# Kernel tuning notes

Measured on AMD Instinct MI355X. Metric: run time of the kernel, lower is better.

The kernel has to match this reference:

```python
import jax, jax.numpy as jnp
import numpy as np

R = 0.9  # compression ratio from init_kwargs


def _dct_matrix(N):
    """Orthonormal DCT-II matrix C of shape [N, N].
    (C @ v) along the last axis equals dct(v, norm='ortho').
    Its transpose is the orthonormal DCT-III (inverse)."""
    n = jnp.arange(N, dtype=jnp.float32)
    k = n[:, None]
    C = jnp.cos(jnp.pi * (2.0 * n[None, :] + 1.0) * k / (2.0 * N))
    s = jnp.full((N,), jnp.sqrt(2.0 / N), dtype=jnp.float32).at[0].set(jnp.sqrt(1.0 / N))
    return s[:, None] * C


def setup_inputs() -> dict:
    key = jax.random.key(0)
    # hidden states [B, T, D]
    x = jax.random.normal(key, (64, 1024, 768), dtype=jnp.float32)
    return {"x": x}


def reference(x):
    """CompressedModel.compress_hidden_state with compress_method='dct' and
    use_compressed_hidden_state=True:
      1) DCT-II (ortho) along the token axis T
      2) keep the first k = ceil(r*T) coefficients
      3) inverse DCT (ortho, size k) to reconstruct a shorter sequence
    Returns (x_reconstructed [B,k,D], x_dct [B,k,D]) matching dc_transform."""
    B, T, D = x.shape
    k = int(np.ceil(R * T))  # static under jit
    C_T = _dct_matrix(T)          # [T, T]
    # DCT along tokens, truncate to low-frequency k coeffs
    x_dct = jnp.einsum('kt,btd->bkd', C_T, x)[:, :k, :]  # [B, k, D]
    # inverse DCT of size k (DCT-III ortho = transpose of DCT-II ortho)
    C_k = _dct_matrix(k)          # [k, k]
    x_rec = jnp.einsum('mn,bmd->bnd', C_k, x_dct)         # [B, k, D]
    return x_rec, x_dct
```

## Files before the change

### kernel.cpp

```cpp
#include <hip/hip_runtime.h>
#include <hip/hip_bf16.h>

typedef __attribute__((ext_vector_type(8))) short short8;
typedef __attribute__((ext_vector_type(4))) float f32x4;

#define T_LEN   1024
#define KKEEP   922
#define DDIM    768
#define NBATCH  64

#define BM 128
#define BN 128
#define BK 32
#define LDSK 40

__global__ void gen_C1(__hip_bfloat16* __restrict__ C1) {
    int idx = blockIdx.x * 256 + threadIdx.x;
    if (idx >= 1024 * 1024) return;
    int kk = idx >> 10;
    int t  = idx & 1023;
    float val = 0.0f;
    if (kk < KKEEP) {
        float a1 = 3.14159265358979323846f * (2.0f * (float)t + 1.0f);
        float a2 = a1 * (float)kk;
        float a3 = a2 / 2048.0f;
        float s  = (kk == 0) ? sqrtf(1.0f / 1024.0f) : sqrtf(2.0f / 1024.0f);
        val = s * cosf(a3);
    }
    C1[idx] = __float2bfloat16(val);
}

__global__ void gen_C2T(__hip_bfloat16* __restrict__ A2) {
    int idx = blockIdx.x * 256 + threadIdx.x;
    if (idx >= 1024 * 928) return;
    int n = idx / 928;
    int m = idx - n * 928;
    float val = 0.0f;
    if (n < KKEEP && m < KKEEP) {
        float a1 = 3.14159265358979323846f * (2.0f * (float)n + 1.0f);
        float a2 = a1 * (float)m;
        float a3 = a2 / 1844.0f;
        float s  = (m == 0) ? sqrtf(1.0f / 922.0f) : sqrtf(2.0f / 922.0f);
        val = s * cosf(a3);
    }
    A2[idx] = __float2bfloat16(val);
}

__global__ __launch_bounds__(256)
void gemm_dct(const __hip_bfloat16* __restrict__ A, int lda, int ksteps,
              const float* __restrict__ B, int bRows, long long bStride,
              float* __restrict__ C, long long cStride)
{
    __shared__ __hip_bfloat16 As[2][BM * LDSK];
    __shared__ __hip_bfloat16 Bs[2][BN * LDSK];

    const int tid   = threadIdx.x;
    const int mBase = blockIdx.y * BM;
    const int nBase = blockIdx.x * BN;

    const float* __restrict__ Bb = B + (long long)blockIdx.z * bStride;
    float* __restrict__       Cb = C + (long long)blockIdx.z * cStride;

    auto stageA = [&](int buf, int k0) {
        int r = tid >> 1, half = tid & 1;
        const uint4* src = (const uint4*)(A + (size_t)(mBase + r) * lda + k0 + half * 16);
        uint4 v0 = src[0], v1 = src[1];
        uint4* dst = (uint4*)&As[buf][r * LDSK + half * 16];
        dst[0] = v0; dst[1] = v1;
    };
    auto stageB = [&](int buf, int k0) {
        #pragma unroll
        for (int p = 0; p < 4; ++p) {
            int idx = p * 256 + tid;
            int k   = idx & 31;
            int n4  = (idx >> 5) * 4;
            int gk  = k0 + k;
            float4 v = make_float4(0.f, 0.f, 0.f, 0.f);
            if (gk < bRows) v = *(const float4*)(Bb + (size_t)gk * DDIM + nBase + n4);
            __hip_bfloat16* d = &Bs[buf][n4 * LDSK + k];
            d[0 * LDSK] = __float2bfloat16(v.x);
            d[1 * LDSK] = __float2bfloat16(v.y);
            d[2 * LDSK] = __float2bfloat16(v.z);
            d[3 * LDSK] = __float2bfloat16(v.w);
        }
    };

    const int lane = tid & 63;
    const int wid  = tid >> 6;
    const int wm   = (wid >> 1) * 64;
    const int wn   = (wid & 1) * 64;
    const int lr   = lane & 15;
    const int g8   = (lane >> 4) * 8;

    f32x4 acc[4][4] = {};

    stageA(0, 0);
    stageB(0, 0);
    __syncthreads();

    for (int s = 0; s < ksteps; ++s) {
        int buf = s & 1;
        if (s + 1 < ksteps) {
            stageA(buf ^ 1, (s + 1) * BK);
            stageB(buf ^ 1, (s + 1) * BK);
        }
        short8 af[4], bfr[4];
        #pragma unroll
        for (int m = 0; m < 4; ++m)
            af[m] = *(const short8*)&As[buf][(wm + m * 16 + lr) * LDSK + g8];
        #pragma unroll
        for (int n = 0; n < 4; ++n)
            bfr[n] = *(const short8*)&Bs[buf][(wn + n * 16 + lr) * LDSK + g8];
        #pragma unroll
        for (int m = 0; m < 4; ++m)
            #pragma unroll
            for (int n = 0; n < 4; ++n)
                acc[m][n] = __builtin_amdgcn_mfma_f32_16x16x32_bf16(af[m], bfr[n], acc[m][n], 0, 0, 0);
        __syncthreads();
    }

    #pragma unroll
    for (int m = 0; m < 4; ++m) {
        int row0 = mBase + wm + m * 16 + (lane >> 4) * 4;
        #pragma unroll
        for (int n = 0; n < 4; ++n) {
            int col = nBase + wn + n * 16 + lr;
            #pragma unroll
            for (int i = 0; i < 4; ++i) {
                int row = row0 + i;
                if (row < KKEEP)
                    Cb[(size_t)row * DDIM + col] = acc[m][n][i];
            }
        }
    }
}

extern "C" void kernel_launch(void* const* d_in, const int* in_sizes, int n_in,
                              void* d_out, int out_size, void* d_ws, size_t ws_size,
                              hipStream_t stream)
{
    const float* x = (const float*)d_in[0];
    float* out  = (float*)d_out;
    float* xrec = out;
    float* xdct = out + (size_t)NBATCH * KKEEP * DDIM;

    __hip_bfloat16* C1 = (__hip_bfloat16*)d_ws;
    __hip_bfloat16* A2 = (__hip_bfloat16*)d_ws + 1024 * 1024;

    gen_C1<<<(1024 * 1024 + 255) / 256, 256, 0, stream>>>(C1);
    gen_C2T<<<(1024 * 928 + 255) / 256, 256, 0, stream>>>(A2);

    dim3 grid(DDIM / BN, 1024 / BM, NBATCH);

    gemm_dct<<<grid, 256, 0, stream>>>(C1, 1024, 32,
                                       x, T_LEN, (long long)T_LEN * DDIM,
                                       xdct, (long long)KKEEP * DDIM);

    gemm_dct<<<grid, 256, 0, stream>>>(A2, 928, 29,
                                       xdct, KKEEP, (long long)KKEEP * DDIM,
                                       xrec, (long long)KKEEP * DDIM);
}
```

Baseline: 976.8 us.

## Pre-transpose inputs to bf16 and use direct global-to-LDS loads in GEMM

Adds a transpose-and-convert kernel that writes x (and xdct when workspace allows) as bf16 in K-contiguous layout, using the xrec output buffer as scratch. A new GEMM then stages both operands with global_load_lds 16-byte transfers into unpadded LDS, replacing the per-element fp32-to-bf16 strided stores inside the main loop. The aim is to cut staging overhead and global traffic in the GEMM, at the price of extra transpose passes. The unpadded LDS layout may also cause bank conflicts.

Measured after the change: 791.0 us. 1.23x faster.

```diff
diff --git a/kernel.cpp b/kernel.cpp
--- a/kernel.cpp
+++ b/kernel.cpp
@@ -9,10 +9,6 @@
 #define DDIM    768
 #define NBATCH  64
 
-#define BM 128
-#define BN 128
-#define BK 32
-#define LDSK 40
 
 __global__ void gen_C1(__hip_bfloat16* __restrict__ C1) {
     int idx = blockIdx.x * 256 + threadIdx.x;
@@ -47,17 +43,124 @@
 }
 
 __global__ __launch_bounds__(256)
+void transpose_cvt(const float* __restrict__ in, __hip_bfloat16* __restrict__ out,
+                   int R, int C, int Rp)
+{
+    __shared__ float tile[64][65];
+    const int r0 = blockIdx.x * 64, c0 = blockIdx.y * 64, z = blockIdx.z;
+    const float* inz = in + (size_t)z * R * C;
+    __hip_bfloat16* outz = out + (size_t)z * C * Rp;
+    const int tid = threadIdx.x;
+    const int lr = tid >> 4, lc4 = (tid & 15) * 4;
+    #pragma unroll
+    for (int i = 0; i < 4; ++i) {
+        int row = i * 16 + lr;
+        int gr  = r0 + row;
+        float4 v = make_float4(0.f, 0.f, 0.f, 0.f);
+        if (gr < R) v = *(const float4*)(inz + (size_t)gr * C + c0 + lc4);
+        tile[row][lc4 + 0] = v.x; tile[row][lc4 + 1] = v.y;
+        tile[row][lc4 + 2] = v.z; tile[row][lc4 + 3] = v.w;
+    }
+    __syncthreads();
+    const int orow = tid >> 2, seg = tid & 3;
+    const int rB = r0 + seg * 16;
+    if (rB < Rp) {
+        alignas(16) __hip_bfloat16 tmp[16];
+        #pragma unroll
+        for (int j = 0; j < 16; ++j)
+            tmp[j] = __float2bfloat16(tile[seg * 16 + j][orow]);
+        uint4* dst = (uint4*)(outz + (size_t)(c0 + orow) * Rp + rB);
+        dst[0] = ((const uint4*)tmp)[0];
+        dst[1] = ((const uint4*)tmp)[1];
+    }
+}
+
+__global__ __launch_bounds__(256)
+void gemm_bf16(const __hip_bfloat16* __restrict__ A, int lda,
+               const __hip_bfloat16* __restrict__ B, int ldb, long long bStride,
+               float* __restrict__ C, long long cStride, int ksteps)
+{
+    __shared__ __hip_bfloat16 As[2][128 * 32];
+    __shared__ __hip_bfloat16 Bs[2][128 * 32];
+
+    const int tid   = threadIdx.x;
+    const int mBase = blockIdx.y * 128;
+    const int nBase = blockIdx.x * 128;
+    const __hip_bfloat16* __restrict__ Bb = B + (long long)blockIdx.z * bStride;
+    float* __restrict__ Cb = C + (long long)blockIdx.z * cStride;
+
+    auto stage = [&](int buf, int k0) {
+        #pragma unroll
+        for (int h = 0; h < 2; ++h) {
+            int c = h * 256 + tid;
+            int row = c >> 2, q = c & 3;
+            const __hip_bfloat16* ga = A + (size_t)(mBase + row) * lda + k0 + q * 8;
+            __builtin_amdgcn_global_load_lds(
+                (const __attribute__((address_space(1))) void*)ga,
+                (__attribute__((address_space(3))) void*)(&As[buf][c * 8]), 16, 0, 0);
+            const __hip_bfloat16* gb = Bb + (size_t)(nBase + row) * ldb + k0 + q * 8;
+            __builtin_amdgcn_global_load_lds(
+                (const __attribute__((address_space(1))) void*)gb,
+                (__attribute__((address_space(3))) void*)(&Bs[buf][c * 8]), 16, 0, 0);
+        }
+    };
+
+    const int lane = tid & 63;
+    const int wid  = tid >> 6;
+    const int wm   = (wid >> 1) * 64;
+    const int wn   = (wid & 1) * 64;
+    const int lr   = lane & 15;
+    const int g8   = (lane >> 4) * 8;
+
+    f32x4 acc[4][4] = {};
+
+    stage(0, 0);
+    for (int s = 0; s < ksteps; ++s) {
+        int buf = s & 1;
+        __syncthreads();
+        if (s + 1 < ksteps) stage(buf ^ 1, (s + 1) * 32);
+        short8 af[4], bfr[4];
+        #pragma unroll
+        for (int m = 0; m < 4; ++m)
+            af[m] = *(const short8*)&As[buf][(wm + m * 16 + lr) * 32 + g8];
+        #pragma unroll
+        for (int n = 0; n < 4; ++n)
+            bfr[n] = *(const short8*)&Bs[buf][(wn + n * 16 + lr) * 32 + g8];
+        #pragma unroll
+        for (int m = 0; m < 4; ++m)
+            #pragma unroll
+            for (int n = 0; n < 4; ++n)
+                acc[m][n] = __builtin_amdgcn_mfma_f32_16x16x32_bf16(af[m], bfr[n], acc[m][n], 0, 0, 0);
+    }
+
+    #pragma unroll
+    for (int m = 0; m < 4; ++m) {
+        int row0 = mBase + wm + m * 16 + (lane >> 4) * 4;
+        #pragma unroll
+        for (int n = 0; n < 4; ++n) {
+            int col = nBase + wn + n * 16 + lr;
+            #pragma unroll
+            for (int i = 0; i < 4; ++i) {
+                int row = row0 + i;
+                if (row < KKEEP)
+                    Cb[(size_t)row * DDIM + col] = acc[m][n][i];
+            }
+        }
+    }
+}
+
+#define BK 32
+#define LDSK 40
+__global__ __launch_bounds__(256)
 void gemm_dct(const __hip_bfloat16* __restrict__ A, int lda, int ksteps,
               const float* __restrict__ B, int bRows, long long bStride,
               float* __restrict__ C, long long cStride)
 {
-    __shared__ __hip_bfloat16 As[2][BM * LDSK];
-    __shared__ __hip_bfloat16 Bs[2][BN * LDSK];
-
+    __shared__ __hip_bfloat16 As[2][128 * LDSK];
+    __shared__ __hip_bfloat16 Bs[2][128 * LDSK];
     const int tid   = threadIdx.x;
-    const int mBase = blockIdx.y * BM;
-    const int nBase = blockIdx.x * BN;
-
+    const int mBase = blockIdx.y * 128;
+    const int nBase = blockIdx.x * 128;
     const float* __restrict__ Bb = B + (long long)blockIdx.z * bStride;
     float* __restrict__       Cb = C + (long long)blockIdx.z * cStride;
 
@@ -91,13 +194,11 @@
     const int wn   = (wid & 1) * 64;
     const int lr   = lane & 15;
     const int g8   = (lane >> 4) * 8;
-
     f32x4 acc[4][4] = {};
 
     stageA(0, 0);
     stageB(0, 0);
     __syncthreads();
-
     for (int s = 0; s < ksteps; ++s) {
         int buf = s & 1;
         if (s + 1 < ksteps) {
@@ -118,7 +219,6 @@
                 acc[m][n] = __builtin_amdgcn_mfma_f32_16x16x32_bf16(af[m], bfr[n], acc[m][n], 0, 0, 0);
         __syncthreads();
     }
-
     #pragma unroll
     for (int m = 0; m < 4; ++m) {
         int row0 = mBase + wm + m * 16 + (lane >> 4) * 4;
@@ -144,19 +244,36 @@
     float* xrec = out;
     float* xdct = out + (size_t)NBATCH * KKEEP * DDIM;
 
+    const size_t SZ_C1  = 1024ull * 1024;
+    const size_t SZ_A2  = 1024ull * 928;
+    const size_t SZ_XDT = 64ull * 768 * 928;
+
     __hip_bfloat16* C1 = (__hip_bfloat16*)d_ws;
-    __hip_bfloat16* A2 = (__hip_bfloat16*)d_ws + 1024 * 1024;
+    __hip_bfloat16* A2 = C1 + SZ_C1;
+    const bool bigws = ws_size >= (SZ_C1 + SZ_A2 + SZ_XDT) * 2;
+    __hip_bfloat16* xdT = A2 + SZ_A2;
+
+    __hip_bfloat16* xT = (__hip_bfloat16*)xrec;
 
     gen_C1<<<(1024 * 1024 + 255) / 256, 256, 0, stream>>>(C1);
     gen_C2T<<<(1024 * 928 + 255) / 256, 256, 0, stream>>>(A2);
 
-    dim3 grid(DDIM / BN, 1024 / BM, NBATCH);
-
-    gemm_dct<<<grid, 256, 0, stream>>>(C1, 1024, 32,
-                                       x, T_LEN, (long long)T_LEN * DDIM,
-                                       xdct, (long long)KKEEP * DDIM);
-
-    gemm_dct<<<grid, 256, 0, stream>>>(A2, 928, 29,
-                                       xdct, KKEEP, (long long)KKEEP * DDIM,
-                                       xrec, (long long)KKEEP * DDIM);
-}
+    transpose_cvt<<<dim3(16, 12, NBATCH), 256, 0, stream>>>(x, xT, 1024, DDIM, 1024);
+
+    dim3 grid(DDIM / 128, 1024 / 128, NBATCH);
+
+    gemm_bf16<<<grid, 256, 0, stream>>>(C1, 1024, xT, 1024,
+                                        (long long)DDIM * 1024,
+                                        xdct, (long long)KKEEP * DDIM, 32);
+
+    if (bigws) {
+        transpose_cvt<<<dim3(15, 12, NBATCH), 256, 0, stream>>>(xdct, xdT, KKEEP, DDIM, 928);
+        gemm_bf16<<<grid, 256, 0, stream>>>(A2, 928, xdT, 928,
+                                            (long long)DDIM * 928,
+                                            xrec, (long long)KKEEP * DDIM, 29);
+    } else {
+        gemm_dct<<<grid, 256, 0, stream>>>(A2, 928, 29,
+                                           xdct, KKEEP, (long long)KKEEP * DDIM,
+                                           xrec, (long long)KKEEP * DDIM);
+    }
+}
```
